# Performance work log

Measured on AMD Instinct MI355X. Metric: run time of the kernel, lower is better.

Reference implementation:

```python
import jax, jax.numpy as jnp
import numpy as np

N = 14        # nodes per graph (fixed by hidden*14 in the Linear)
H = 4         # attention heads
F_IN = 128    # num_feature
C = 64        # hidden (per-head out_channels; concat=False -> mean over heads)
NEG_SLOPE = 0.2  # PyG GATConv default negative_slope


def gat_conv(x, src, dst, W, a_src, a_dst, b):
    """One PyG-style GATConv on a single graph.
    x: [N, F]  W: [F, H*C]  a_src/a_dst: [H, C]  b: [C]
    src/dst: [E] int (self-loops already appended). concat=False -> mean over heads.
    """
    h = (x @ W).reshape(N, H, C)                       # [N,H,C]
    al_src = jnp.einsum('nhc,hc->nh', h, a_src)        # [N,H]
    al_dst = jnp.einsum('nhc,hc->nh', h, a_dst)        # [N,H]
    e = jax.nn.leaky_relu(al_src[src] + al_dst[dst], NEG_SLOPE)  # [E,H]
    # softmax over incoming edges of each destination node (stable)
    m = jax.ops.segment_max(e, dst, num_segments=N)    # [N,H]
    ex = jnp.exp(e - m[dst])
    denom = jax.ops.segment_sum(ex, dst, num_segments=N)
    alpha = ex / denom[dst]                            # [E,H]
    out = jax.ops.segment_sum(alpha[:, :, None] * h[src], dst, num_segments=N)  # [N,H,C]
    return out.mean(axis=1) + b                        # [N,C]


def setup_inputs() -> dict:
    key = jax.random.key(0)
    ks = jax.random.split(key, 12)
    B, E = 16384, 182
    feature = jax.random.normal(ks[0], (B, N, F_IN), dtype=jnp.float32)
    edge_list = jax.random.randint(ks[1], (B, E, 2), 0, N, dtype=jnp.int64)

    def glorot(k, shape):
        fan = shape[0] + shape[-1]
        return jax.random.normal(k, shape, dtype=jnp.float32) * jnp.sqrt(2.0 / fan)

    return {
        'feature': feature,
        'edge_list': edge_list,
        'W1': glorot(ks[2], (F_IN, H * C)),
        'a_src1': glorot(ks[3], (H, C)),
        'a_dst1': glorot(ks[4], (H, C)),
        'b1': jnp.zeros((C,), jnp.float32),
        'W2': glorot(ks[5], (C, H * C)),
        'a_src2': glorot(ks[6], (H, C)),
        'a_dst2': glorot(ks[7], (H, C)),
        'b2': jnp.zeros((C,), jnp.float32),
        'W_lin': glorot(ks[8], (N * C, C // 2)),
        'b_lin': jnp.zeros((C // 2,), jnp.float32),
        'W_pred': glorot(ks[9], (C // 2, 1)),
        'b_pred': jnp.zeros((1,), jnp.float32),
    }


def reference(feature, edge_list, W1, a_src1, a_dst1, b1, W2, a_src2, a_dst2, b2,
              W_lin, b_lin, W_pred, b_pred):
    B = feature.shape[0]
    # PyG GATConv adds self-loops by default
    loops = jnp.broadcast_to(jnp.arange(N, dtype=edge_list.dtype), (B, N))
    src = jnp.concatenate([edge_list[..., 0], loops], axis=1)  # [B, E+N]
    dst = jnp.concatenate([edge_list[..., 1], loops], axis=1)

    def per_graph(x, s, d):
        h = jax.nn.relu(gat_conv(x, s, d, W1, a_src1, a_dst1, b1))
        # dropout is identity in eval mode
        h = gat_conv(h, s, d, W2, a_src2, a_dst2, b2)       # [N,C]
        z = h.reshape(-1) @ W_lin + b_lin                    # [C//2]
        p = z @ W_pred + b_pred                              # [1]
        return jax.nn.sigmoid(p)

    return jax.vmap(per_graph)(feature, src, dst)            # [B,1]
```

## Files before the change

### kernel.cpp

```cpp
#include <hip/hip_runtime.h>

#define NN 14
#define HH 4
#define CC 64
#define FF 128
#define EE 182

typedef __attribute__((ext_vector_type(8))) short bf16x8;
typedef __attribute__((ext_vector_type(4))) float f32x4;
typedef __attribute__((ext_vector_type(4))) unsigned u32x4;

__device__ __forceinline__ unsigned f2bf(float f) {
    unsigned u = __float_as_uint(f);
    return (u + 0x7fffu + ((u >> 16) & 1u)) >> 16;
}
__device__ __forceinline__ unsigned pack2bf(float lo, float hi) {
    return __builtin_amdgcn_perm(__float_as_uint(hi) + 0x8000u,
                                 __float_as_uint(lo) + 0x8000u, 0x07060302u);
}
__device__ __forceinline__ bf16x8 mk8(unsigned a, unsigned b, unsigned c, unsigned d) {
    u32x4 u = {a, b, c, d};
    return __builtin_bit_cast(bf16x8, u);
}

__global__ void prep_pack(const float* __restrict__ W1, const float* __restrict__ W2,
                          const float* __restrict__ Wl, const float* __restrict__ Wpred,
                          const float* __restrict__ bl, const float* __restrict__ bp,
                          const float* __restrict__ as1, const float* __restrict__ ad1,
                          const float* __restrict__ as2, const float* __restrict__ ad2,
                          short* __restrict__ wp1, short* __restrict__ wp2,
                          short* __restrict__ battn1, short* __restrict__ battn2,
                          float* __restrict__ wcomb) {
    int gid = blockIdx.x * 256 + threadIdx.x;
    if (gid < 32768) {
        int j = gid & 7, L = (gid >> 3) & 63, kk = (gid >> 9) & 3, nt = gid >> 11;
        int k = kk * 32 + (L >> 4) * 8 + j, n = nt * 16 + (L & 15);
        wp1[gid] = (short)f2bf(W1[k * 256 + n]);
    } else if (gid < 49152) {
        int g2 = gid - 32768;
        int j = g2 & 7, L = (g2 >> 3) & 63, kk = (g2 >> 9) & 1, nt = g2 >> 10;
        int k = kk * 32 + (L >> 4) * 8 + j, n = nt * 16 + (L & 15);
        wp2[g2] = (short)f2bf(W2[k * 256 + n]);
    } else if (gid < 51200) {
        int g2 = gid - 49152;
        int j = g2 & 7, L = (g2 >> 3) & 63, kk = g2 >> 9;
        int n = L & 15, k = kk * 32 + (L >> 4) * 8 + j;
        float val = 0.f;
        if (n < 8) {
            const float* av = ((n >> 2) ? ad1 : as1) + (n & 3) * 64;
            const float* wr = W1 + k * 256 + (n & 3) * 64;
            for (int c = 0; c < 64; ++c) val += wr[c] * av[c];
        }
        battn1[g2] = (short)f2bf(val);
    } else if (gid < 52224) {
        int g2 = gid - 51200;
        int j = g2 & 7, L = (g2 >> 3) & 63, kk = g2 >> 9;
        int n = L & 15, k = kk * 32 + (L >> 4) * 8 + j;
        float val = 0.f;
        if (n < 8) {
            const float* av = ((n >> 2) ? ad2 : as2) + (n & 3) * 64;
            const float* wr = W2 + k * 256 + (n & 3) * 64;
            for (int c = 0; c < 64; ++c) val += wr[c] * av[c];
        }
        battn2[g2] = (short)f2bf(val);
    } else if (gid < 53120) {
        int i = gid - 52224;
        const float* wr = Wl + i * 32;
        float acc = 0.f;
        #pragma unroll
        for (int j = 0; j < 32; ++j) acc += wr[j] * Wpred[j];
        wcomb[i] = acc;
    } else if (gid == 53120) {
        float acc = bp[0];
        #pragma unroll
        for (int j = 0; j < 32; ++j) acc += bl[j] * Wpred[j];
        wcomb[896] = acc;
    }
}

template<int KK, bool RELU>
__device__ __forceinline__ void gat_layer(int lane,
    const bf16x8* a, const short* wpB,
    const float* __restrict__ bias,
    const float* cntf, const float* alsd,
    f32x4* o, unsigned (*po)[2])
{
    const int m = lane & 15, q = lane >> 4;
    f32x4 agg[4];
    #pragma unroll
    for (int ct = 0; ct < 4; ++ct) agg[ct] = f32x4{0.f, 0.f, 0.f, 0.f};

    #pragma unroll
    for (int hp = 0; hp < 2; ++hp) {
        unsigned hb[8][2];
        #pragma unroll
        for (int hsub = 0; hsub < 2; ++hsub) {
            f32x4 c[4];
            #pragma unroll
            for (int ct = 0; ct < 4; ++ct) c[ct] = f32x4{0.f, 0.f, 0.f, 0.f};
            #pragma unroll
            for (int ct = 0; ct < 4; ++ct)
                #pragma unroll
                for (int kk = 0; kk < KK; ++kk) {
                    bf16x8 b = *(const bf16x8*)(wpB +
                        ((((hp * 2 + hsub) * 4 + ct) * KK + kk) * 64 + lane) * 8);
                    c[ct] = __builtin_amdgcn_mfma_f32_16x16x32_bf16(a[kk], b, c[ct], 0, 0, 0);
                }
            #pragma unroll
            for (int ct = 0; ct < 4; ++ct) {
                hb[hsub * 4 + ct][0] = pack2bf(c[ct][0], c[ct][1]);
                hb[hsub * 4 + ct][1] = pack2bf(c[ct][2], c[ct][3]);
            }
        }

        const int hh = hp * 2 + (q >> 1);
        const float myald = alsd[64 + hh * 16 + m];
        const float* asrc = alsd + hh * 16 + (q & 1) * 8;
        const float* csrc = cntf + m * 20 + (q & 1) * 8;
        f32x4 aL = *(const f32x4*)asrc, aH = *(const f32x4*)(asrc + 4);
        f32x4 cL = *(const f32x4*)csrc, cH = *(const f32x4*)(csrc + 4);
        float v[8], s8 = 0.f;
        #pragma unroll
        for (int j = 0; j < 8; ++j) {
            float l = ((j < 4) ? aL[j] : aH[j - 4]) + myald;
            l = fmaxf(l, 0.f) + 0.2f * fminf(l, 0.f);
            float e = __expf(l) * ((j < 4) ? cL[j] : cH[j - 4]);
            v[j] = e; s8 += e;
        }
        s8 += __shfl_xor(s8, 16);
        float inv = (s8 > 0.f) ? 0.25f / s8 : 0.f;
        bf16x8 P = mk8(pack2bf(v[0] * inv, v[1] * inv), pack2bf(v[2] * inv, v[3] * inv),
                       pack2bf(v[4] * inv, v[5] * inv), pack2bf(v[6] * inv, v[7] * inv));

        #pragma unroll
        for (int ct = 0; ct < 4; ++ct) {
            unsigned aw[4];
            #pragma unroll
            for (int jj = 0; jj < 4; ++jj) {
                int srcl = ((q & 1) * 2 + (jj >> 1)) * 16 + m;
                unsigned aE = __shfl((int)hb[ct][jj & 1], srcl);
                unsigned aO = __shfl((int)hb[4 + ct][jj & 1], srcl);
                aw[jj] = (q >> 1) ? aO : aE;
            }
            agg[ct] = __builtin_amdgcn_mfma_f32_16x16x32_bf16(
                mk8(aw[0], aw[1], aw[2], aw[3]), P, agg[ct], 0, 0, 0);
        }
    }

    #pragma unroll
    for (int ct = 0; ct < 4; ++ct) {
        float4 bb = *(const float4*)(bias + ct * 16 + q * 4);
        float o0 = agg[ct][0] + bb.x, o1 = agg[ct][1] + bb.y;
        float o2 = agg[ct][2] + bb.z, o3 = agg[ct][3] + bb.w;
        if (RELU) {
            o0 = fmaxf(o0, 0.f); o1 = fmaxf(o1, 0.f);
            o2 = fmaxf(o2, 0.f); o3 = fmaxf(o3, 0.f);
            if (m >= NN) { o0 = 0.f; o1 = 0.f; o2 = 0.f; o3 = 0.f; }
            po[ct][0] = pack2bf(o0, o1);
            po[ct][1] = pack2bf(o2, o3);
        } else {
            o[ct] = f32x4{o0, o1, o2, o3};
        }
    }
}

__global__ __launch_bounds__(1024, 4) void gat_fused(
    const float* __restrict__ feature,
    const int*   __restrict__ edge_list,
    const float* __restrict__ b1, const float* __restrict__ b2,
    const short* __restrict__ wpck,
    const float* __restrict__ wcomb,
    float* __restrict__ out, int B)
{
    const int w = threadIdx.x >> 6, lane = threadIdx.x & 63;
    const int m = lane & 15, q = lane >> 4;

    __shared__ __align__(16) short swts[52224];
    __shared__ __align__(16) unsigned slab[16 * 448];

    float* cntf = (float*)(slab + w * 448);
    float* alsd = (float*)(slab + w * 448 + 320);

    {
        const u32x4* srcw = (const u32x4*)wpck;
        u32x4* dstw = (u32x4*)swts;
        #pragma unroll
        for (int r = 0; r < 7; ++r) {
            int i = r * 1024 + (int)threadIdx.x;
            if (i < 6528) dstw[i] = srcw[i];
        }
    }
    __syncthreads();

    const short* swp1  = swts;
    const short* swp2  = swts + 32768;
    const short* sbat1 = swts + 49152;
    const short* sbat2 = swts + 51200;

    const int g0 = blockIdx.x * 64 + w * 4;

    #pragma clang loop unroll(disable)
    for (int it = 0; it < 4; ++it) {
        const int g = g0 + it;
        if (g >= B) break;

        #pragma unroll
        for (int i = 0; i < 5; ++i) cntf[i * 64 + lane] = 0.f;
        {
            const int2* ep = (const int2*)edge_list + (size_t)g * EE;
            #pragma unroll
            for (int r = 0; r < 3; ++r) {
                int i = r * 64 + lane;
                if (i < EE) { int2 e = ep[i]; atomicAdd(&cntf[e.y * 20 + e.x], 1.f); }
            }
            if (lane < NN) atomicAdd(&cntf[lane * 21], 1.f);
        }

        bf16x8 a1[4];
        #pragma unroll
        for (int kk = 0; kk < 4; ++kk) a1[kk] = mk8(0, 0, 0, 0);
        if (m < NN) {
            const float* xg = feature + (size_t)g * (NN * FF) + m * FF;
            #pragma unroll
            for (int kk = 0; kk < 4; ++kk) {
                float4 v0 = *(const float4*)(xg + kk * 32 + q * 8);
                float4 v1 = *(const float4*)(xg + kk * 32 + q * 8 + 4);
                a1[kk] = mk8(pack2bf(v0.x, v0.y), pack2bf(v0.z, v0.w),
                             pack2bf(v1.x, v1.y), pack2bf(v1.z, v1.w));
            }
        }

        {
            f32x4 ca = f32x4{0.f, 0.f, 0.f, 0.f};
            #pragma unroll
            for (int kk = 0; kk < 4; ++kk) {
                bf16x8 b = *(const bf16x8*)(sbat1 + (kk * 64 + lane) * 8);
                ca = __builtin_amdgcn_mfma_f32_16x16x32_bf16(a1[kk], b, ca, 0, 0, 0);
            }
            if (m < 8) *(f32x4*)(alsd + (m >> 2) * 64 + (m & 3) * 16 + q * 4) = ca;
        }

        unsigned po1[4][2];
        gat_layer<4, true>(lane, a1, swp1, b1, cntf, alsd, nullptr, po1);

        bf16x8 a2[2];
        #pragma unroll
        for (int kk = 0; kk < 2; ++kk) {
            unsigned wv[4];
            #pragma unroll
            for (int j2 = 0; j2 < 4; ++j2) {
                int srcl = ((q & 1) * 2 + (j2 >> 1)) * 16 + m;
                unsigned vE = __shfl((int)po1[2 * kk][j2 & 1], srcl);
                unsigned vO = __shfl((int)po1[2 * kk + 1][j2 & 1], srcl);
                wv[j2] = (q >> 1) ? vO : vE;
            }
            a2[kk] = mk8(wv[0], wv[1], wv[2], wv[3]);
        }

        {
            f32x4 ca = f32x4{0.f, 0.f, 0.f, 0.f};
            #pragma unroll
            for (int kk = 0; kk < 2; ++kk) {
                bf16x8 b = *(const bf16x8*)(sbat2 + (kk * 64 + lane) * 8);
                ca = __builtin_amdgcn_mfma_f32_16x16x32_bf16(a2[kk], b, ca, 0, 0, 0);
            }
            if (m < 8) *(f32x4*)(alsd + (m >> 2) * 64 + (m & 3) * 16 + q * 4) = ca;
        }

        f32x4 o2[4];
        gat_layer<2, false>(lane, a2, swp2, b2, cntf, alsd, o2, nullptr);

        float p = 0.f;
        if (m < NN) {
            const float* wc = wcomb + m * 64 + q * 4;
            #pragma unroll
            for (int ct = 0; ct < 4; ++ct) {
                float4 w4 = *(const float4*)(wc + ct * 16);
                p += o2[ct][0] * w4.x + o2[ct][1] * w4.y +
                     o2[ct][2] * w4.z + o2[ct][3] * w4.w;
            }
        }
        p += __shfl_xor(p, 1);  p += __shfl_xor(p, 2);  p += __shfl_xor(p, 4);
        p += __shfl_xor(p, 8);  p += __shfl_xor(p, 16); p += __shfl_xor(p, 32);
        if (lane == 0) out[g] = 1.f / (1.f + __expf(-(p + wcomb[896])));
    }
}

extern "C" void kernel_launch(void* const* d_in, const int* in_sizes, int n_in,
                              void* d_out, int out_size, void* d_ws, size_t ws_size,
                              hipStream_t stream) {
    const float* feature = (const float*)d_in[0];
    const int*   edges   = (const int*)d_in[1];
    const float* W1  = (const float*)d_in[2];
    const float* as1 = (const float*)d_in[3];
    const float* ad1 = (const float*)d_in[4];
    const float* b1  = (const float*)d_in[5];
    const float* W2  = (const float*)d_in[6];
    const float* as2 = (const float*)d_in[7];
    const float* ad2 = (const float*)d_in[8];
    const float* b2  = (const float*)d_in[9];
    const float* Wl  = (const float*)d_in[10];
    const float* bl  = (const float*)d_in[11];
    const float* Wp  = (const float*)d_in[12];
    const float* bp  = (const float*)d_in[13];
    float* out = (float*)d_out;

    short* wp1    = (short*)d_ws;
    short* wp2    = wp1 + 32768;
    short* battn1 = wp2 + 16384;
    short* battn2 = battn1 + 2048;
    float* wcomb  = (float*)(battn2 + 1024);

    prep_pack<<<208, 256, 0, stream>>>(W1, W2, Wl, Wp, bl, bp, as1, ad1, as2, ad2,
                                       wp1, wp2, battn1, battn2, wcomb);

    const int B = in_sizes[0] / (NN * FF);
    gat_fused<<<(B + 63) / 64, 1024, 0, stream>>>(feature, edges, b1, b2,
                                                  wp1, wcomb, out, B);
}
```

Baseline: 240.3 us.

## Restructure per-head aggregation with 16x16x16 MFMA and stage layer output via LDS

Each head is now processed on its own: the attention weights form the A operand of a 16x16x16 bf16 MFMA, which removes the cross-lane shuffles previously used to transpose head features. The layer-1 output goes through a per-wave fp32 LDS scratch to build the layer-2 A operand instead of using shuffles. Layer-1 weights are read straight from global memory rather than staged in LDS, which cuts LDS weight storage while adding per-wave scratch. The combined linear-prediction weights are transposed to match the new output layout. The trade-off is more global or L2 traffic for W1 and extra LDS writes and reads, in exchange for fewer shuffles and possibly different occupancy.

```diff
diff --git a/kernel.cpp b/kernel.cpp
--- a/kernel.cpp
+++ b/kernel.cpp
@@ -1,14 +1,13 @@
 #include <hip/hip_runtime.h>
 
 #define NN 14
-#define HH 4
-#define CC 64
-#define FF 128
 #define EE 182
 
 typedef __attribute__((ext_vector_type(8))) short bf16x8;
+typedef __attribute__((ext_vector_type(4))) short bf16x4;
 typedef __attribute__((ext_vector_type(4))) float f32x4;
 typedef __attribute__((ext_vector_type(4))) unsigned u32x4;
+typedef __attribute__((ext_vector_type(2))) unsigned u32x2;
 
 __device__ __forceinline__ unsigned f2bf(float f) {
     unsigned u = __float_as_uint(f);
@@ -21,6 +20,10 @@
 __device__ __forceinline__ bf16x8 mk8(unsigned a, unsigned b, unsigned c, unsigned d) {
     u32x4 u = {a, b, c, d};
     return __builtin_bit_cast(bf16x8, u);
+}
+__device__ __forceinline__ bf16x4 mk4(unsigned a, unsigned b) {
+    u32x2 u = {a, b};
+    return __builtin_bit_cast(bf16x4, u);
 }
 
 __global__ void prep_pack(const float* __restrict__ W1, const float* __restrict__ W2,
@@ -30,7 +33,7 @@
                           const float* __restrict__ as2, const float* __restrict__ ad2,
                           short* __restrict__ wp1, short* __restrict__ wp2,
                           short* __restrict__ battn1, short* __restrict__ battn2,
-                          float* __restrict__ wcomb) {
+                          float* __restrict__ wcombT) {
     int gid = blockIdx.x * 256 + threadIdx.x;
     if (gid < 32768) {
         int j = gid & 7, L = (gid >> 3) & 63, kk = (gid >> 9) & 3, nt = gid >> 11;
@@ -63,18 +66,21 @@
             for (int c = 0; c < 64; ++c) val += wr[c] * av[c];
         }
         battn2[g2] = (short)f2bf(val);
-    } else if (gid < 53120) {
-        int i = gid - 52224;
-        const float* wr = Wl + i * 32;
+    } else if (gid < 53248) {
+        int o = gid - 52224;
+        int n = o & 15, c = o >> 4;
         float acc = 0.f;
-        #pragma unroll
-        for (int j = 0; j < 32; ++j) acc += wr[j] * Wpred[j];
-        wcomb[i] = acc;
-    } else if (gid == 53120) {
+        if (n < NN) {
+            const float* wr = Wl + (n * 64 + c) * 32;
+            #pragma unroll
+            for (int j = 0; j < 32; ++j) acc += wr[j] * Wpred[j];
+        }
+        wcombT[o] = acc;
+    } else if (gid == 53248) {
         float acc = bp[0];
         #pragma unroll
         for (int j = 0; j < 32; ++j) acc += bl[j] * Wpred[j];
-        wcomb[896] = acc;
+        wcombT[1024] = acc;
     }
 }
 
@@ -83,7 +89,7 @@
     const bf16x8* a, const short* wpB,
     const float* __restrict__ bias,
     const float* cntf, const float* alsd,
-    f32x4* o, unsigned (*po)[2])
+    float* x2f, f32x4* o)
 {
     const int m = lane & 15, q = lane >> 4;
     f32x4 agg[4];
@@ -91,75 +97,59 @@
     for (int ct = 0; ct < 4; ++ct) agg[ct] = f32x4{0.f, 0.f, 0.f, 0.f};
 
     #pragma unroll
-    for (int hp = 0; hp < 2; ++hp) {
-        unsigned hb[8][2];
-        #pragma unroll
-        for (int hsub = 0; hsub < 2; ++hsub) {
-            f32x4 c[4];
-            #pragma unroll
-            for (int ct = 0; ct < 4; ++ct) c[ct] = f32x4{0.f, 0.f, 0.f, 0.f};
-            #pragma unroll
-            for (int ct = 0; ct < 4; ++ct)
-                #pragma unroll
-                for (int kk = 0; kk < KK; ++kk) {
-                    bf16x8 b = *(const bf16x8*)(wpB +
-                        ((((hp * 2 + hsub) * 4 + ct) * KK + kk) * 64 + lane) * 8);
-                    c[ct] = __builtin_amdgcn_mfma_f32_16x16x32_bf16(a[kk], b, c[ct], 0, 0, 0);
-                }
-            #pragma unroll
-            for (int ct = 0; ct < 4; ++ct) {
-                hb[hsub * 4 + ct][0] = pack2bf(c[ct][0], c[ct][1]);
-                hb[hsub * 4 + ct][1] = pack2bf(c[ct][2], c[ct][3]);
-            }
-        }
-
-        const int hh = hp * 2 + (q >> 1);
-        const float myald = alsd[64 + hh * 16 + m];
-        const float* asrc = alsd + hh * 16 + (q & 1) * 8;
-        const float* csrc = cntf + m * 20 + (q & 1) * 8;
-        f32x4 aL = *(const f32x4*)asrc, aH = *(const f32x4*)(asrc + 4);
-        f32x4 cL = *(const f32x4*)csrc, cH = *(const f32x4*)(csrc + 4);
-        float v[8], s8 = 0.f;
-        #pragma unroll
-        for (int j = 0; j < 8; ++j) {
-            float l = ((j < 4) ? aL[j] : aH[j - 4]) + myald;
-            l = fmaxf(l, 0.f) + 0.2f * fminf(l, 0.f);
-            float e = __expf(l) * ((j < 4) ? cL[j] : cH[j - 4]);
-            v[j] = e; s8 += e;
-        }
-        s8 += __shfl_xor(s8, 16);
-        float inv = (s8 > 0.f) ? 0.25f / s8 : 0.f;
-        bf16x8 P = mk8(pack2bf(v[0] * inv, v[1] * inv), pack2bf(v[2] * inv, v[3] * inv),
-                       pack2bf(v[4] * inv, v[5] * inv), pack2bf(v[6] * inv, v[7] * inv));
-
+    for (int h = 0; h < 4; ++h) {
+        unsigned hf[4][2];
         #pragma unroll
         for (int ct = 0; ct < 4; ++ct) {
-            unsigned aw[4];
-            #pragma unroll
-            for (int jj = 0; jj < 4; ++jj) {
-                int srcl = ((q & 1) * 2 + (jj >> 1)) * 16 + m;
-                unsigned aE = __shfl((int)hb[ct][jj & 1], srcl);
-                unsigned aO = __shfl((int)hb[4 + ct][jj & 1], srcl);
-                aw[jj] = (q >> 1) ? aO : aE;
-            }
-            agg[ct] = __builtin_amdgcn_mfma_f32_16x16x32_bf16(
-                mk8(aw[0], aw[1], aw[2], aw[3]), P, agg[ct], 0, 0, 0);
-        }
+            f32x4 c = f32x4{0.f, 0.f, 0.f, 0.f};
+            #pragma unroll
+            for (int kk = 0; kk < KK; ++kk) {
+                bf16x8 b = *(const bf16x8*)(wpB +
+                    (((h * 4 + ct) * KK + kk) * 64 + lane) * 8);
+                c = __builtin_amdgcn_mfma_f32_16x16x32_bf16(a[kk], b, c, 0, 0, 0);
+            }
+            hf[ct][0] = pack2bf(c[0], c[1]);
+            hf[ct][1] = pack2bf(c[2], c[3]);
+        }
+
+        f32x4 alv = *(const f32x4*)(alsd + h * 16 + q * 4);
+        float ad  = alsd[64 + h * 16 + m];
+        f32x4 cv  = *(const f32x4*)(cntf + m * 20 + q * 4);
+        float v0, v1, v2, v3;
+        {
+            float l0 = alv[0] + ad, l1 = alv[1] + ad, l2 = alv[2] + ad, l3 = alv[3] + ad;
+            l0 = fmaxf(l0, 0.f) + 0.2f * fminf(l0, 0.f);
+            l1 = fmaxf(l1, 0.f) + 0.2f * fminf(l1, 0.f);
+            l2 = fmaxf(l2, 0.f) + 0.2f * fminf(l2, 0.f);
+            l3 = fmaxf(l3, 0.f) + 0.2f * fminf(l3, 0.f);
+            v0 = __expf(l0) * cv[0]; v1 = __expf(l1) * cv[1];
+            v2 = __expf(l2) * cv[2]; v3 = __expf(l3) * cv[3];
+        }
+        float s = v0 + v1 + v2 + v3;
+        s += __shfl_xor(s, 16);
+        s += __shfl_xor(s, 32);
+        float inv = (s > 0.f) ? 0.25f / s : 0.f;
+        bf16x4 P = mk4(pack2bf(v0 * inv, v1 * inv), pack2bf(v2 * inv, v3 * inv));
+
+        #pragma unroll
+        for (int ct = 0; ct < 4; ++ct)
+            agg[ct] = __builtin_amdgcn_mfma_f32_16x16x16bf16_1k(
+                P, mk4(hf[ct][0], hf[ct][1]), agg[ct], 0, 0, 0);
     }
 
     #pragma unroll
     for (int ct = 0; ct < 4; ++ct) {
-        float4 bb = *(const float4*)(bias + ct * 16 + q * 4);
-        float o0 = agg[ct][0] + bb.x, o1 = agg[ct][1] + bb.y;
-        float o2 = agg[ct][2] + bb.z, o3 = agg[ct][3] + bb.w;
+        float bb = bias[ct * 16 + m];
         if (RELU) {
-            o0 = fmaxf(o0, 0.f); o1 = fmaxf(o1, 0.f);
-            o2 = fmaxf(o2, 0.f); o3 = fmaxf(o3, 0.f);
-            if (m >= NN) { o0 = 0.f; o1 = 0.f; o2 = 0.f; o3 = 0.f; }
-            po[ct][0] = pack2bf(o0, o1);
-            po[ct][1] = pack2bf(o2, o3);
+            #pragma unroll
+            for (int r = 0; r < 4; ++r) {
+                float v = fmaxf(agg[ct][r] + bb, 0.f);
+                if (q * 4 + r >= NN) v = 0.f;
+                x2f[(q * 4 + r) * 68 + ct * 16 + m] = v;
+            }
         } else {
-            o[ct] = f32x4{o0, o1, o2, o3};
+            o[ct] = f32x4{agg[ct][0] + bb, agg[ct][1] + bb,
+                          agg[ct][2] + bb, agg[ct][3] + bb};
         }
     }
 }
@@ -168,34 +158,36 @@
     const float* __restrict__ feature,
     const int*   __restrict__ edge_list,
     const float* __restrict__ b1, const float* __restrict__ b2,
+    const short* __restrict__ wp1,
     const short* __restrict__ wpck,
-    const float* __restrict__ wcomb,
+    const float* __restrict__ wcombT,
     float* __restrict__ out, int B)
 {
     const int w = threadIdx.x >> 6, lane = threadIdx.x & 63;
     const int m = lane & 15, q = lane >> 4;
 
-    __shared__ __align__(16) short swts[52224];
+    __shared__ __align__(16) short    swts[19456];
     __shared__ __align__(16) unsigned slab[16 * 448];
+    __shared__ __align__(16) float    x2f_all[16 * 1088];
 
     float* cntf = (float*)(slab + w * 448);
     float* alsd = (float*)(slab + w * 448 + 320);
+    float* x2f  = x2f_all + w * 1088;
 
     {
         const u32x4* srcw = (const u32x4*)wpck;
         u32x4* dstw = (u32x4*)swts;
         #pragma unroll
-        for (int r = 0; r < 7; ++r) {
+        for (int r = 0; r < 3; ++r) {
             int i = r * 1024 + (int)threadIdx.x;
-            if (i < 6528) dstw[i] = srcw[i];
+            if (i < 2432) dstw[i] = srcw[i];
         }
     }
     __syncthreads();
 
-    const short* swp1  = swts;
-    const short* swp2  = swts + 32768;
-    const short* sbat1 = swts + 49152;
-    const short* sbat2 = swts + 51200;
+    const short* swp2  = swts;
+    const short* sbat1 = swts + 16384;
+    const short* sbat2 = swts + 18432;
 
     const int g0 = blockIdx.x * 64 + w * 4;
 
@@ -220,7 +212,7 @@
         #pragma unroll
         for (int kk = 0; kk < 4; ++kk) a1[kk] = mk8(0, 0, 0, 0);
         if (m < NN) {
-            const float* xg = feature + (size_t)g * (NN * FF) + m * FF;
+            const float* xg = feature + (size_t)g * (NN * 128) + m * 128;
             #pragma unroll
             for (int kk = 0; kk < 4; ++kk) {
                 float4 v0 = *(const float4*)(xg + kk * 32 + q * 8);
@@ -240,21 +232,15 @@
             if (m < 8) *(f32x4*)(alsd + (m >> 2) * 64 + (m & 3) * 16 + q * 4) = ca;
         }
 
-        unsigned po1[4][2];
-        gat_layer<4, true>(lane, a1, swp1, b1, cntf, alsd, nullptr, po1);
+        gat_layer<4, true>(lane, a1, wp1, b1, cntf, alsd, x2f, nullptr);
 
         bf16x8 a2[2];
         #pragma unroll
         for (int kk = 0; kk < 2; ++kk) {
-            unsigned wv[4];
-            #pragma unroll
-            for (int j2 = 0; j2 < 4; ++j2) {
-                int srcl = ((q & 1) * 2 + (j2 >> 1)) * 16 + m;
-                unsigned vE = __shfl((int)po1[2 * kk][j2 & 1], srcl);
-                unsigned vO = __shfl((int)po1[2 * kk + 1][j2 & 1], srcl);
-                wv[j2] = (q >> 1) ? vO : vE;
-            }
-            a2[kk] = mk8(wv[0], wv[1], wv[2], wv[3]);
+            f32x4 lo = *(const f32x4*)(x2f + m * 68 + kk * 32 + q * 8);
+            f32x4 hi = *(const f32x4*)(x2f + m * 68 + kk * 32 + q * 8 + 4);
+            a2[kk] = mk8(pack2bf(lo[0], lo[1]), pack2bf(lo[2], lo[3]),
+                         pack2bf(hi[0], hi[1]), pack2bf(hi[2], hi[3]));
         }
 
         {
@@ -268,21 +254,18 @@
         }
 
         f32x4 o2[4];
-        gat_layer<2, false>(lane, a2, swp2, b2, cntf, alsd, o2, nullptr);
+        gat_layer<2, false>(lane, a2, swp2, b2, cntf, alsd, nullptr, o2);
 
         float p = 0.f;
-        if (m < NN) {
-            const float* wc = wcomb + m * 64 + q * 4;
-            #pragma unroll
-            for (int ct = 0; ct < 4; ++ct) {
-                float4 w4 = *(const float4*)(wc + ct * 16);
-                p += o2[ct][0] * w4.x + o2[ct][1] * w4.y +
-                     o2[ct][2] * w4.z + o2[ct][3] * w4.w;
-            }
+        #pragma unroll
+        for (int ct = 0; ct < 4; ++ct) {
+            float4 wv = *(const float4*)(wcombT + (ct * 16 + m) * 16 + q * 4);
+            p += o2[ct][0] * wv.x + o2[ct][1] * wv.y +
+                 o2[ct][2] * wv.z + o2[ct][3] * wv.w;
         }
         p += __shfl_xor(p, 1);  p += __shfl_xor(p, 2);  p += __shfl_xor(p, 4);
         p += __shfl_xor(p, 8);  p += __shfl_xor(p, 16); p += __shfl_xor(p, 32);
-        if (lane == 0) out[g] = 1.f / (1.f + __expf(-(p + wcomb[896])));
+        if (lane == 0) out[g] = 1.f / (1.f + __expf(-(p + wcombT[1024])));
     }
 }
 
@@ -309,12 +292,12 @@
     short* wp2    = wp1 + 32768;
     short* battn1 = wp2 + 16384;
     short* battn2 = battn1 + 2048;
-    float* wcomb  = (float*)(battn2 + 1024);
-
-    prep_pack<<<208, 256, 0, stream>>>(W1, W2, Wl, Wp, bl, bp, as1, ad1, as2, ad2,
-                                       wp1, wp2, battn1, battn2, wcomb);
-
-    const int B = in_sizes[0] / (NN * FF);
+    float* wcombT = (float*)(battn2 + 1024);
+
+    prep_pack<<<209, 256, 0, stream>>>(W1, W2, Wl, Wp, bl, bp, as1, ad1, as2, ad2,
+                                       wp1, wp2, battn1, battn2, wcombT);
+
+    const int B = in_sizes[0] / (NN * 128);
     gat_fused<<<(B + 63) / 64, 1024, 0, stream>>>(feature, edges, b1, b2,
-                                                  wp1, wcomb, out, B);
-}
+                                                  wp1, wp2, wcombT, out, B);
+}
```

Result: slower. 342.9 us (+42.7%).
